# Optimization experiments

Measured on AMD Instinct MI355X. Metric: run time of the kernel, lower is better.

The kernel has to match this reference:

```python
import jax, jax.numpy as jnp
import numpy as np

N = 100000      # nodes
E = 800000      # edges
D_IN = 128
H = 4           # heads
C = 32          # out channels per head (out_feature = H*C = 128)
EPS = 1e-5


def setup_inputs() -> dict:
    key = jax.random.key(0)
    ks = jax.random.split(key, 12)
    x = jax.random.normal(ks[0], (N, D_IN), dtype=jnp.float32)
    edge_index = jax.random.randint(ks[1], (2, E), 0, N, dtype=jnp.int32)
    edge_weights = jax.random.uniform(ks[2], (E, 1), dtype=jnp.float32)
    s = 1.0 / np.sqrt(D_IN)
    W_l = jax.random.uniform(ks[3], (D_IN, H * C), jnp.float32, -s, s)   # GATv2 lin_l (source)
    W_r = jax.random.uniform(ks[4], (D_IN, H * C), jnp.float32, -s, s)   # GATv2 lin_r (target)
    W_e = jax.random.uniform(ks[5], (1, H * C), jnp.float32, -1.0, 1.0)  # lin_edge (edge_dim=1)
    att = jax.random.uniform(ks[6], (H, C), jnp.float32, -s, s)          # attention vector
    bias = jnp.zeros((H * C,), jnp.float32)
    gamma = jnp.ones((H * C,), jnp.float32)   # BatchNorm weight
    beta = jnp.zeros((H * C,), jnp.float32)   # BatchNorm bias
    return {"x": x, "edge_index": edge_index, "edge_weights": edge_weights,
            "W_l": W_l, "W_r": W_r, "W_e": W_e, "att": att, "bias": bias,
            "gamma": gamma, "beta": beta}


def reference(x, edge_index, edge_weights, W_l, W_r, W_e, att, bias, gamma, beta):
    src = edge_index[0]  # message source j
    dst = edge_index[1]  # message target i (aggregation index)

    x_l = (x @ W_l).reshape(N, H, C)
    x_r = (x @ W_r).reshape(N, H, C)
    e = (edge_weights @ W_e).reshape(E, H, C)

    # GATv2 message: LeakyReLU(x_j + x_i + e, 0.2), score = <att, .>
    xj = x_l[src]                                  # [E,H,C]
    m = jax.nn.leaky_relu(xj + x_r[dst] + e, 0.2)  # [E,H,C]
    logits = jnp.einsum('ehc,hc->eh', m, att)      # [E,H]

    # segment softmax over edges sharing the same destination
    seg_max = jax.ops.segment_max(logits, dst, num_segments=N)  # [N,H]
    seg_max = jnp.where(jnp.isfinite(seg_max), seg_max, 0.0)
    expv = jnp.exp(logits - seg_max[dst])
    seg_sum = jax.ops.segment_sum(expv, dst, num_segments=N)
    alpha = expv / (seg_sum[dst] + 1e-16)          # [E,H]

    out = jax.ops.segment_sum(xj * alpha[:, :, None], dst, num_segments=N)  # [N,H,C]
    out = out.reshape(N, H * C) + bias

    # BatchNorm1d over nodes (training-mode batch statistics, biased var)
    mu = jnp.mean(out, axis=0)
    var = jnp.var(out, axis=0)
    out = gamma * (out - mu) * jax.lax.rsqrt(var + EPS) + beta

    # F.leaky_relu default negative_slope=0.01; dropout is identity in eval
    return jax.nn.leaky_relu(out, 0.01)
```

## Files before the change

### kernel.cpp

```cpp
#include <hip/hip_runtime.h>

#define D 128

typedef __bf16 v8bf __attribute__((ext_vector_type(8)));
typedef float v4f __attribute__((ext_vector_type(4)));

__device__ __forceinline__ unsigned short f2bfbits(float f) {
    unsigned u = __float_as_uint(f);
    u += 0x7FFFu + ((u >> 16) & 1u);
    return (unsigned short)(u >> 16);
}

__device__ __forceinline__ float4 ldbf4(const __bf16* p) {
    const uint2 u = *reinterpret_cast<const uint2*>(p);
    float4 r;
    r.x = __uint_as_float(u.x << 16);
    r.y = __uint_as_float(u.x & 0xFFFF0000u);
    r.z = __uint_as_float(u.y << 16);
    r.w = __uint_as_float(u.y & 0xFFFF0000u);
    return r;
}

__global__ __launch_bounds__(256) void wprep_zero_k(
    const float* __restrict__ Wl, const float* __restrict__ Wr,
    __bf16* __restrict__ Wbf, int* __restrict__ zbase, int zcount) {
    if ((int)blockIdx.x < 128) {
        const int i = blockIdx.x * 256 + threadIdx.x;
        const int cg = i >> 7;
        const int k = i & 127;
        const float* __restrict__ Wp = (cg < D) ? Wl : Wr;
        Wbf[i] = (__bf16)Wp[(size_t)k * D + (cg & (D - 1))];
        return;
    }
    const int i = ((int)blockIdx.x - 128) * 256 + threadIdx.x;
    if (i < zcount) zbase[i] = 0;
}

__global__ __launch_bounds__(256, 1) void gemm_deg_k(
    const float* __restrict__ x, const __bf16* __restrict__ Wbf,
    __bf16* __restrict__ xl, __bf16* __restrict__ xr, int n, int nTiles,
    int gemmGrid, const int* __restrict__ dst, int* __restrict__ deg,
    unsigned char* __restrict__ rank, int E) {
    if ((int)blockIdx.x >= gemmGrid) {
        const int e = ((int)blockIdx.x - gemmGrid) * 256 + threadIdx.x;
        if (e < E) rank[e] = (unsigned char)atomicAdd(&deg[dst[e]], 1);
        return;
    }
    __shared__ __align__(16) unsigned short xs[64][136];
    const int tid = threadIdx.x;
    const int lane = tid & 63;
    const int wid = tid >> 6;
    const int col16 = lane & 15;
    const int kg = lane >> 4;

    v8bf bfr[4][4];
#pragma unroll
    for (int nt = 0; nt < 4; ++nt) {
        const int cg = (wid * 4 + nt) * 16 + col16;
#pragma unroll
        for (int ks = 0; ks < 4; ++ks)
            bfr[nt][ks] = *reinterpret_cast<const v8bf*>(
                &Wbf[(size_t)cg * 128 + ks * 32 + kg * 8]);
    }

    v8bf pre[4];
    int tile = (int)blockIdx.x;
    {
        const int row0 = tile * 64;
#pragma unroll
        for (int j = 0; j < 4; ++j) {
            const int i = tid + j * 256;
            const int row = row0 + (i >> 4);
            const int k0 = (i & 15) * 8;
            float4 v0 = make_float4(0.f, 0.f, 0.f, 0.f), v1 = v0;
            if (row < n) {
                v0 = *reinterpret_cast<const float4*>(&x[(size_t)row * D + k0]);
                v1 = *reinterpret_cast<const float4*>(&x[(size_t)row * D + k0 + 4]);
            }
            v8bf t;
            t[0] = (__bf16)v0.x; t[1] = (__bf16)v0.y;
            t[2] = (__bf16)v0.z; t[3] = (__bf16)v0.w;
            t[4] = (__bf16)v1.x; t[5] = (__bf16)v1.y;
            t[6] = (__bf16)v1.z; t[7] = (__bf16)v1.w;
            pre[j] = t;
        }
    }

    while (tile < nTiles) {
        const int row0 = tile * 64;
#pragma unroll
        for (int j = 0; j < 4; ++j) {
            const int i = tid + j * 256;
            *reinterpret_cast<v8bf*>(&xs[i >> 4][(i & 15) * 8]) = pre[j];
        }
        __syncthreads();

        const int next = tile + gemmGrid;
        if (next < nTiles) {
            const int nrow0 = next * 64;
#pragma unroll
            for (int j = 0; j < 4; ++j) {
                const int i = tid + j * 256;
                const int row = nrow0 + (i >> 4);
                const int k0 = (i & 15) * 8;
                float4 v0 = make_float4(0.f, 0.f, 0.f, 0.f), v1 = v0;
                if (row < n) {
                    v0 = *reinterpret_cast<const float4*>(&x[(size_t)row * D + k0]);
                    v1 = *reinterpret_cast<const float4*>(&x[(size_t)row * D + k0 + 4]);
                }
                v8bf t;
                t[0] = (__bf16)v0.x; t[1] = (__bf16)v0.y;
                t[2] = (__bf16)v0.z; t[3] = (__bf16)v0.w;
                t[4] = (__bf16)v1.x; t[5] = (__bf16)v1.y;
                t[6] = (__bf16)v1.z; t[7] = (__bf16)v1.w;
                pre[j] = t;
            }
        }

        v4f acc[4][4] = {};
#pragma unroll
        for (int mt = 0; mt < 4; ++mt) {
            v8bf afr[4];
#pragma unroll
            for (int ks = 0; ks < 4; ++ks)
                afr[ks] = *reinterpret_cast<const v8bf*>(
                    &xs[mt * 16 + col16][ks * 32 + kg * 8]);
#pragma unroll
            for (int nt = 0; nt < 4; ++nt)
#pragma unroll
                for (int ks = 0; ks < 4; ++ks)
                    acc[mt][nt] = __builtin_amdgcn_mfma_f32_16x16x32_bf16(
                        bfr[nt][ks], afr[ks], acc[mt][nt], 0, 0, 0);
        }
#pragma unroll
        for (int mt = 0; mt < 4; ++mt) {
            const int row = row0 + mt * 16 + col16;
            if (row < n) {
#pragma unroll
                for (int nt = 0; nt < 4; ++nt) {
                    const int cgb = (wid * 4 + nt) * 16 + kg * 4;
                    __bf16* __restrict__ op = (cgb < D) ? xl : xr;
                    const int c = cgb & (D - 1);
                    uint2 pkt;
                    pkt.x = ((unsigned)f2bfbits(acc[mt][nt][1]) << 16) |
                            f2bfbits(acc[mt][nt][0]);
                    pkt.y = ((unsigned)f2bfbits(acc[mt][nt][3]) << 16) |
                            f2bfbits(acc[mt][nt][2]);
                    *reinterpret_cast<uint2*>(&op[(size_t)row * D + c]) = pkt;
                }
            }
        }
        __syncthreads();
        tile = next;
    }
}

__global__ __launch_bounds__(256) void scan_k(
    const int* __restrict__ deg, int* __restrict__ rowptr,
    int* __restrict__ scanctr, int n) {
    __shared__ int tmp[256];
    __shared__ int sbase;
    const int i = blockIdx.x * 256 + threadIdx.x;
    const int v = (i < n) ? deg[i] : 0;
    tmp[threadIdx.x] = v;
    __syncthreads();
    for (int off = 1; off < 256; off <<= 1) {
        int t = (threadIdx.x >= off) ? tmp[threadIdx.x - off] : 0;
        __syncthreads();
        tmp[threadIdx.x] += t;
        __syncthreads();
    }
    if (threadIdx.x == 255) sbase = atomicAdd(scanctr, tmp[255]);
    __syncthreads();
    if (i < n) rowptr[i] = sbase + tmp[threadIdx.x] - v;
}

__global__ __launch_bounds__(256) void fill_k(
    const int* __restrict__ src, const int* __restrict__ dst,
    const float* __restrict__ ew, const int* __restrict__ rowptr,
    const unsigned char* __restrict__ rank, int2* __restrict__ epay,
    int E, int n) {
    const int xcd = blockIdx.x & 7;
    const int nchunk = gridDim.x >> 3;
    const int slice = (n + 7) >> 3;
    const int lo = xcd * slice;
    const int hi = min(n, lo + slice);
    const int stride = nchunk * 256;
    for (int e = ((int)blockIdx.x >> 3) * 256 + threadIdx.x; e < E; e += stride) {
        const int d = dst[e];
        if (d >= lo && d < hi) {
            const int p = rowptr[d] + (int)rank[e];
            int2 v;
            v.x = src[e];
            v.y = __float_as_int(ew[e]);
            epay[p] = v;
        }
    }
}

__global__ __launch_bounds__(256) void node_aggr_k(
    const __bf16* __restrict__ xl, const __bf16* __restrict__ xr,
    const int2* __restrict__ epay, const int* __restrict__ rowptr,
    const int* __restrict__ deg, const float* __restrict__ We,
    const float* __restrict__ att, __bf16* __restrict__ outb, int n) {
    const int wgl = (int)((blockIdx.x * (size_t)blockDim.x + threadIdx.x) >> 6);
    const int lane = threadIdx.x & 63;
    const int half = lane >> 5;
    const int node = wgl * 2 + half;
    const int ch = (lane & 31) * 4;

    int beg = 0, dg = 0;
    if (node < n) {
        beg = rowptr[node];
        dg = deg[node];
    }
    const int end = beg + dg;
    const int tmax = max(dg, __shfl_xor(dg, 32));

    float4 b = make_float4(0.f, 0.f, 0.f, 0.f);
    if (node < n) b = ldbf4(&xr[(size_t)node * D + ch]);
    const float4 we4 = *reinterpret_cast<const float4*>(&We[ch]);
    const float4 at4 = *reinterpret_cast<const float4*>(&att[ch]);

    float s = 0.f;
    float4 acc = make_float4(0.f, 0.f, 0.f, 0.f);
    for (int t = 0; t < tmax; t += 4) {
        float part[4];
        float4 av[4];
#pragma unroll
        for (int i = 0; i < 4; ++i) {
            const int p = beg + t + i;
            const int q = max(min(p, end - 1), 0);
            const int2 pw = epay[q];
            av[i] = ldbf4(&xl[(size_t)pw.x * D + ch]);
            const float wgt = __int_as_float(pw.y);
            float c0 = fmaf(wgt, we4.x, av[i].x + b.x);
            float c1 = fmaf(wgt, we4.y, av[i].y + b.y);
            float c2 = fmaf(wgt, we4.z, av[i].z + b.z);
            float c3 = fmaf(wgt, we4.w, av[i].w + b.w);
            c0 = fmaxf(c0, 0.2f * c0);
            c1 = fmaxf(c1, 0.2f * c1);
            c2 = fmaxf(c2, 0.2f * c2);
            c3 = fmaxf(c3, 0.2f * c3);
            part[i] = fmaf(c3, at4.w, fmaf(c2, at4.z, fmaf(c1, at4.y, c0 * at4.x)));
        }
#pragma unroll
        for (int off = 1; off < 8; off <<= 1) {
            part[0] += __shfl_xor(part[0], off);
            part[1] += __shfl_xor(part[1], off);
            part[2] += __shfl_xor(part[2], off);
            part[3] += __shfl_xor(part[3], off);
        }
        const float pv0 = (t + 0 < dg) ? __expf(fminf(part[0], 50.f)) : 0.f;
        const float pv1 = (t + 1 < dg) ? __expf(fminf(part[1], 50.f)) : 0.f;
        const float pv2 = (t + 2 < dg) ? __expf(fminf(part[2], 50.f)) : 0.f;
        const float pv3 = (t + 3 < dg) ? __expf(fminf(part[3], 50.f)) : 0.f;
        s += (pv0 + pv1) + (pv2 + pv3);
        acc.x += fmaf(pv3, av[3].x, fmaf(pv2, av[2].x,
                 fmaf(pv1, av[1].x, pv0 * av[0].x)));
        acc.y += fmaf(pv3, av[3].y, fmaf(pv2, av[2].y,
                 fmaf(pv1, av[1].y, pv0 * av[0].y)));
        acc.z += fmaf(pv3, av[3].z, fmaf(pv2, av[2].z,
                 fmaf(pv1, av[1].z, pv0 * av[0].z)));
        acc.w += fmaf(pv3, av[3].w, fmaf(pv2, av[2].w,
                 fmaf(pv1, av[1].w, pv0 * av[0].w)));
    }
    if (node < n) {
        const float inv = 1.f / (s + 1e-16f);
        uint2 pkt;
        pkt.x = ((unsigned)f2bfbits(acc.y * inv) << 16) | f2bfbits(acc.x * inv);
        pkt.y = ((unsigned)f2bfbits(acc.w * inv) << 16) | f2bfbits(acc.z * inv);
        *reinterpret_cast<uint2*>(&outb[(size_t)node * D + ch]) = pkt;
    }
}

__global__ __launch_bounds__(256) void bn_partial_k(
    const __bf16* __restrict__ outb, float* __restrict__ sums,
    float* __restrict__ sumsq, int n) {
    __shared__ float rs[8][128];
    __shared__ float rq[8][128];
    const int c4 = (threadIdx.x & 31) * 4;
    const int rstr = threadIdx.x >> 5;
    float4 s = make_float4(0.f, 0.f, 0.f, 0.f);
    float4 q = make_float4(0.f, 0.f, 0.f, 0.f);
    for (int r = blockIdx.x * 8 + rstr; r < n; r += gridDim.x * 8) {
        const float4 v = ldbf4(&outb[(size_t)r * D + c4]);
        s.x += v.x; s.y += v.y; s.z += v.z; s.w += v.w;
        q.x = fmaf(v.x, v.x, q.x);
        q.y = fmaf(v.y, v.y, q.y);
        q.z = fmaf(v.z, v.z, q.z);
        q.w = fmaf(v.w, v.w, q.w);
    }
    rs[rstr][c4 + 0] = s.x; rs[rstr][c4 + 1] = s.y;
    rs[rstr][c4 + 2] = s.z; rs[rstr][c4 + 3] = s.w;
    rq[rstr][c4 + 0] = q.x; rq[rstr][c4 + 1] = q.y;
    rq[rstr][c4 + 2] = q.z; rq[rstr][c4 + 3] = q.w;
    __syncthreads();
    const int t = threadIdx.x;
    if (t < 128) {
        float a = 0.f;
#pragma unroll
        for (int j = 0; j < 8; ++j) a += rs[j][t];
        atomicAdd(&sums[t], a);
    } else {
        const int c = t - 128;
        float a = 0.f;
#pragma unroll
        for (int j = 0; j < 8; ++j) a += rq[j][c];
        atomicAdd(&sumsq[c], a);
    }
}

__global__ __launch_bounds__(256) void bn_apply_k(
    const __bf16* __restrict__ outb, float* __restrict__ out,
    const float* __restrict__ bnsums, const float* __restrict__ gamma,
    const float* __restrict__ beta, int n, int total4) {
    const int i = blockIdx.x * blockDim.x + threadIdx.x;
    if (i >= total4) return;
    const int c4 = (i & 31) * 4;
    const float inv_n = 1.f / (float)n;
    const float4 sm = *reinterpret_cast<const float4*>(&bnsums[c4]);
    const float4 sq = *reinterpret_cast<const float4*>(&bnsums[D + c4]);
    const float4 g = *reinterpret_cast<const float4*>(&gamma[c4]);
    const float4 bt = *reinterpret_cast<const float4*>(&beta[c4]);
    float4 v = ldbf4(&outb[(size_t)i * 4]);
    float mu, var, scale, shift, r;
    mu = sm.x * inv_n; var = fmaxf(sq.x * inv_n - mu * mu, 0.f);
    scale = g.x * rsqrtf(var + 1e-5f); shift = bt.x - mu * scale;
    r = fmaf(v.x, scale, shift); v.x = fmaxf(r, 0.01f * r);
    mu = sm.y * inv_n; var = fmaxf(sq.y * inv_n - mu * mu, 0.f);
    scale = g.y * rsqrtf(var + 1e-5f); shift = bt.y - mu * scale;
    r = fmaf(v.y, scale, shift); v.y = fmaxf(r, 0.01f * r);
    mu = sm.z * inv_n; var = fmaxf(sq.z * inv_n - mu * mu, 0.f);
    scale = g.z * rsqrtf(var + 1e-5f); shift = bt.z - mu * scale;
    r = fmaf(v.z, scale, shift); v.z = fmaxf(r, 0.01f * r);
    mu = sm.w * inv_n; var = fmaxf(sq.w * inv_n - mu * mu, 0.f);
    scale = g.w * rsqrtf(var + 1e-5f); shift = bt.w - mu * scale;
    r = fmaf(v.w, scale, shift); v.w = fmaxf(r, 0.01f * r);
    *reinterpret_cast<float4*>(&out[(size_t)i * 4]) = v;
}

extern "C" void kernel_launch(void* const* d_in, const int* in_sizes, int n_in,
                              void* d_out, int out_size, void* d_ws, size_t ws_size,
                              hipStream_t stream) {
    const float* x     = (const float*)d_in[0];
    const int*   ei    = (const int*)d_in[1];
    const float* ew    = (const float*)d_in[2];
    const float* Wl    = (const float*)d_in[3];
    const float* Wr    = (const float*)d_in[4];
    const float* We    = (const float*)d_in[5];
    const float* att   = (const float*)d_in[6];
    const float* gamma = (const float*)d_in[8];
    const float* beta  = (const float*)d_in[9];

    const int n = in_sizes[0] / D;
    const int E = in_sizes[2];
    const int* src = ei;
    const int* dst = ei + E;
    const int nblk = (n + 255) / 256;

    char* ws = (char*)d_ws;
    size_t off = 0;
    __bf16* xl = (__bf16*)(ws + off);   off += (size_t)n * D * 2;
    __bf16* xr = (__bf16*)(ws + off);   off += (size_t)n * D * 2;
    __bf16* outb = (__bf16*)(ws + off); off += (size_t)n * D * 2;
    __bf16* Wbf = (__bf16*)(ws + off);  off += (size_t)2 * D * D * 2;
    float* bnsums = (float*)(ws + off); off += 2 * D * sizeof(float);
    int* scanctr = (int*)(ws + off);    off += 4 * sizeof(int);
    int* deg = (int*)(ws + off);        off += (size_t)n * sizeof(int);
    int* rowptr = (int*)(ws + off);     off += ((size_t)n + 1) * sizeof(int);
    unsigned char* rank = (unsigned char*)(ws + off); off += (size_t)E;
    off = (off + 15) & ~(size_t)15;
    int2* epay = (int2*)(ws + off);     off += (size_t)E * sizeof(int2);

    float* outacc = (float*)d_out;

    const int zcount = 2 * D + 4 + n;
    const int zblocks = (zcount + 255) / 256;

    wprep_zero_k<<<128 + zblocks, 256, 0, stream>>>(Wl, Wr, Wbf,
                                                    (int*)bnsums, zcount);

    const int nTiles = (n + 63) / 64;
    const int gemmGrid = 512;
    const int degBlocks = (E + 255) / 256;
    gemm_deg_k<<<gemmGrid + degBlocks, 256, 0, stream>>>(
        x, Wbf, xl, xr, n, nTiles, gemmGrid, dst, deg, rank, E);

    scan_k<<<nblk, 256, 0, stream>>>(deg, rowptr, scanctr, n);

    fill_k<<<2048, 256, 0, stream>>>(src, dst, ew, rowptr, rank, epay, E, n);

    const int waves = (n + 1) / 2;
    node_aggr_k<<<(waves + 3) / 4, 256, 0, stream>>>(xl, xr, epay, rowptr,
                                                     deg, We, att, outb, n);

    bn_partial_k<<<512, 256, 0, stream>>>(outb, bnsums, bnsums + D, n);
    bn_apply_k<<<((n * D / 4) + 255) / 256, 256, 0, stream>>>(
        outb, outacc, bnsums, gamma, beta, n, n * D / 4);
}
```

Before: 171.1 us.

## Split degree counters into eight sub-histograms to cut atomic contention

The degree counting atomics now target one of eight per-block-group copies of the degree array, selected by block index. The scan kernel sums the eight copies into a total, writes rowptr and deg, and replaces each sub-counter with its exclusive offset. The fill kernel then finds each edge's slot through the matching sub-offset. This aims to reduce atomic collisions on shared counters, at the cost of zeroing, reading and writing eight times more counter memory and scattering the atomics across a larger footprint.

```diff
diff --git a/kernel.cpp b/kernel.cpp
--- a/kernel.cpp
+++ b/kernel.cpp
@@ -39,11 +39,15 @@
 __global__ __launch_bounds__(256, 1) void gemm_deg_k(
     const float* __restrict__ x, const __bf16* __restrict__ Wbf,
     __bf16* __restrict__ xl, __bf16* __restrict__ xr, int n, int nTiles,
-    int gemmGrid, const int* __restrict__ dst, int* __restrict__ deg,
+    int gemmGrid, const int* __restrict__ dst, int* __restrict__ deg8,
     unsigned char* __restrict__ rank, int E) {
     if ((int)blockIdx.x >= gemmGrid) {
-        const int e = ((int)blockIdx.x - gemmGrid) * 256 + threadIdx.x;
-        if (e < E) rank[e] = (unsigned char)atomicAdd(&deg[dst[e]], 1);
+        const int f = (int)blockIdx.x - gemmGrid;
+        const int e = f * 256 + threadIdx.x;
+        if (e < E) {
+            const int sub = f & 7;
+            rank[e] = (unsigned char)atomicAdd(&deg8[(size_t)sub * n + dst[e]], 1);
+        }
         return;
     }
     __shared__ __align__(16) unsigned short xs[64][136];
@@ -156,13 +160,21 @@
 }
 
 __global__ __launch_bounds__(256) void scan_k(
-    const int* __restrict__ deg, int* __restrict__ rowptr,
+    int* __restrict__ deg8, int* __restrict__ deg, int* __restrict__ rowptr,
     int* __restrict__ scanctr, int n) {
     __shared__ int tmp[256];
     __shared__ int sbase;
     const int i = blockIdx.x * 256 + threadIdx.x;
-    const int v = (i < n) ? deg[i] : 0;
-    tmp[threadIdx.x] = v;
+    int d8[8];
+    int total = 0;
+    if (i < n) {
+#pragma unroll
+        for (int s = 0; s < 8; ++s) {
+            d8[s] = deg8[(size_t)s * n + i];
+            total += d8[s];
+        }
+    }
+    tmp[threadIdx.x] = total;
     __syncthreads();
     for (int off = 1; off < 256; off <<= 1) {
         int t = (threadIdx.x >= off) ? tmp[threadIdx.x - off] : 0;
@@ -172,12 +184,21 @@
     }
     if (threadIdx.x == 255) sbase = atomicAdd(scanctr, tmp[255]);
     __syncthreads();
-    if (i < n) rowptr[i] = sbase + tmp[threadIdx.x] - v;
+    if (i < n) {
+        int base = sbase + tmp[threadIdx.x] - total;
+        rowptr[i] = base;
+        deg[i] = total;
+#pragma unroll
+        for (int s = 0; s < 8; ++s) {
+            deg8[(size_t)s * n + i] = base;
+            base += d8[s];
+        }
+    }
 }
 
 __global__ __launch_bounds__(256) void fill_k(
     const int* __restrict__ src, const int* __restrict__ dst,
-    const float* __restrict__ ew, const int* __restrict__ rowptr,
+    const float* __restrict__ ew, const int* __restrict__ off8,
     const unsigned char* __restrict__ rank, int2* __restrict__ epay,
     int E, int n) {
     const int xcd = blockIdx.x & 7;
@@ -189,7 +210,8 @@
     for (int e = ((int)blockIdx.x >> 3) * 256 + threadIdx.x; e < E; e += stride) {
         const int d = dst[e];
         if (d >= lo && d < hi) {
-            const int p = rowptr[d] + (int)rank[e];
+            const int sub = (e >> 8) & 7;
+            const int p = off8[(size_t)sub * n + d] + (int)rank[e];
             int2 v;
             v.x = src[e];
             v.y = __float_as_int(ew[e]);
@@ -367,6 +389,7 @@
     __bf16* Wbf = (__bf16*)(ws + off);  off += (size_t)2 * D * D * 2;
     float* bnsums = (float*)(ws + off); off += 2 * D * sizeof(float);
     int* scanctr = (int*)(ws + off);    off += 4 * sizeof(int);
+    int* deg8 = (int*)(ws + off);       off += (size_t)8 * n * sizeof(int);
     int* deg = (int*)(ws + off);        off += (size_t)n * sizeof(int);
     int* rowptr = (int*)(ws + off);     off += ((size_t)n + 1) * sizeof(int);
     unsigned char* rank = (unsigned char*)(ws + off); off += (size_t)E;
@@ -375,7 +398,7 @@
 
     float* outacc = (float*)d_out;
 
-    const int zcount = 2 * D + 4 + n;
+    const int zcount = 2 * D + 4 + 8 * n;
     const int zblocks = (zcount + 255) / 256;
 
     wprep_zero_k<<<128 + zblocks, 256, 0, stream>>>(Wl, Wr, Wbf,
@@ -385,11 +408,11 @@
     const int gemmGrid = 512;
     const int degBlocks = (E + 255) / 256;
     gemm_deg_k<<<gemmGrid + degBlocks, 256, 0, stream>>>(
-        x, Wbf, xl, xr, n, nTiles, gemmGrid, dst, deg, rank, E);
-
-    scan_k<<<nblk, 256, 0, stream>>>(deg, rowptr, scanctr, n);
-
-    fill_k<<<2048, 256, 0, stream>>>(src, dst, ew, rowptr, rank, epay, E, n);
+        x, Wbf, xl, xr, n, nTiles, gemmGrid, dst, deg8, rank, E);
+
+    scan_k<<<nblk, 256, 0, stream>>>(deg8, deg, rowptr, scanctr, n);
+
+    fill_k<<<2048, 256, 0, stream>>>(src, dst, ew, deg8, rank, epay, E, n);
 
     const int waves = (n + 1) / 2;
     node_aggr_k<<<(waves + 3) / 4, 256, 0, stream>>>(xl, xr, epay, rowptr,
```

After: 171.5 us. No clear change (+0.3%).

## Load GEMM A fragments directly from global, one tile per block

Applied to the files above, without the earlier changes.

The persistent 512-block GEMM loop, with LDS staging and register prefetch of the next tile, is replaced by one 64-row tile per block. Each lane now reads its A-fragment straight from global fp32 x and converts it to bf16 in registers, so there is no shared memory and no barriers. This drops the LDS round trip and synchronisation and lets the hardware scheduler overlap blocks. In exchange, each block reloads the W fragments (many more blocks now), and the global reads of x are strided per lane rather than fully coalesced.

```diff
diff --git a/kernel.cpp b/kernel.cpp
--- a/kernel.cpp
+++ b/kernel.cpp
@@ -39,19 +39,19 @@
 __global__ __launch_bounds__(256, 1) void gemm_deg_k(
     const float* __restrict__ x, const __bf16* __restrict__ Wbf,
     __bf16* __restrict__ xl, __bf16* __restrict__ xr, int n, int nTiles,
-    int gemmGrid, const int* __restrict__ dst, int* __restrict__ deg,
+    const int* __restrict__ dst, int* __restrict__ deg,
     unsigned char* __restrict__ rank, int E) {
-    if ((int)blockIdx.x >= gemmGrid) {
-        const int e = ((int)blockIdx.x - gemmGrid) * 256 + threadIdx.x;
+    if ((int)blockIdx.x >= nTiles) {
+        const int e = ((int)blockIdx.x - nTiles) * 256 + threadIdx.x;
         if (e < E) rank[e] = (unsigned char)atomicAdd(&deg[dst[e]], 1);
         return;
     }
-    __shared__ __align__(16) unsigned short xs[64][136];
     const int tid = threadIdx.x;
     const int lane = tid & 63;
     const int wid = tid >> 6;
     const int col16 = lane & 15;
     const int kg = lane >> 4;
+    const int row0 = blockIdx.x * 64;
 
     v8bf bfr[4][4];
 #pragma unroll
@@ -63,95 +63,49 @@
                 &Wbf[(size_t)cg * 128 + ks * 32 + kg * 8]);
     }
 
-    v8bf pre[4];
-    int tile = (int)blockIdx.x;
-    {
-        const int row0 = tile * 64;
-#pragma unroll
-        for (int j = 0; j < 4; ++j) {
-            const int i = tid + j * 256;
-            const int row = row0 + (i >> 4);
-            const int k0 = (i & 15) * 8;
-            float4 v0 = make_float4(0.f, 0.f, 0.f, 0.f), v1 = v0;
-            if (row < n) {
-                v0 = *reinterpret_cast<const float4*>(&x[(size_t)row * D + k0]);
-                v1 = *reinterpret_cast<const float4*>(&x[(size_t)row * D + k0 + 4]);
-            }
+    v4f acc[4][4] = {};
+#pragma unroll
+    for (int mt = 0; mt < 4; ++mt) {
+        const int row = row0 + mt * 16 + col16;
+        const float* __restrict__ xp = &x[(size_t)min(row, n - 1) * D];
+        v8bf afr[4];
+#pragma unroll
+        for (int ks = 0; ks < 4; ++ks) {
+            const int k0 = ks * 32 + kg * 8;
+            const float4 v0 = *reinterpret_cast<const float4*>(&xp[k0]);
+            const float4 v1 = *reinterpret_cast<const float4*>(&xp[k0 + 4]);
             v8bf t;
             t[0] = (__bf16)v0.x; t[1] = (__bf16)v0.y;
             t[2] = (__bf16)v0.z; t[3] = (__bf16)v0.w;
             t[4] = (__bf16)v1.x; t[5] = (__bf16)v1.y;
             t[6] = (__bf16)v1.z; t[7] = (__bf16)v1.w;
-            pre[j] = t;
-        }
-    }
-
-    while (tile < nTiles) {
-        const int row0 = tile * 64;
-#pragma unroll
-        for (int j = 0; j < 4; ++j) {
-            const int i = tid + j * 256;
-            *reinterpret_cast<v8bf*>(&xs[i >> 4][(i & 15) * 8]) = pre[j];
-        }
-        __syncthreads();
-
-        const int next = tile + gemmGrid;
-        if (next < nTiles) {
-            const int nrow0 = next * 64;
-#pragma unroll
-            for (int j = 0; j < 4; ++j) {
-                const int i = tid + j * 256;
-                const int row = nrow0 + (i >> 4);
-                const int k0 = (i & 15) * 8;
-                float4 v0 = make_float4(0.f, 0.f, 0.f, 0.f), v1 = v0;
-                if (row < n) {
-                    v0 = *reinterpret_cast<const float4*>(&x[(size_t)row * D + k0]);
-                    v1 = *reinterpret_cast<const float4*>(&x[(size_t)row * D + k0 + 4]);
-                }
-                v8bf t;
-                t[0] = (__bf16)v0.x; t[1] = (__bf16)v0.y;
-                t[2] = (__bf16)v0.z; t[3] = (__bf16)v0.w;
-                t[4] = (__bf16)v1.x; t[5] = (__bf16)v1.y;
-                t[6] = (__bf16)v1.z; t[7] = (__bf16)v1.w;
-                pre[j] = t;
+            afr[ks] = t;
+        }
+#pragma unroll
+        for (int nt = 0; nt < 4; ++nt)
+#pragma unroll
+            for (int ks = 0; ks < 4; ++ks)
+                acc[mt][nt] = __builtin_amdgcn_mfma_f32_16x16x32_bf16(
+                    bfr[nt][ks], afr[ks], acc[mt][nt], 0, 0, 0);
+    }
+
+#pragma unroll
+    for (int mt = 0; mt < 4; ++mt) {
+        const int row = row0 + mt * 16 + col16;
+        if (row < n) {
+#pragma unroll
+            for (int nt = 0; nt < 4; ++nt) {
+                const int cgb = (wid * 4 + nt) * 16 + kg * 4;
+                __bf16* __restrict__ op = (cgb < D) ? xl : xr;
+                const int c = cgb & (D - 1);
+                uint2 pkt;
+                pkt.x = ((unsigned)f2bfbits(acc[mt][nt][1]) << 16) |
+                        f2bfbits(acc[mt][nt][0]);
+                pkt.y = ((unsigned)f2bfbits(acc[mt][nt][3]) << 16) |
+                        f2bfbits(acc[mt][nt][2]);
+                *reinterpret_cast<uint2*>(&op[(size_t)row * D + c]) = pkt;
             }
         }
-
-        v4f acc[4][4] = {};
-#pragma unroll
-        for (int mt = 0; mt < 4; ++mt) {
-            v8bf afr[4];
-#pragma unroll
-            for (int ks = 0; ks < 4; ++ks)
-                afr[ks] = *reinterpret_cast<const v8bf*>(
-                    &xs[mt * 16 + col16][ks * 32 + kg * 8]);
-#pragma unroll
-            for (int nt = 0; nt < 4; ++nt)
-#pragma unroll
-                for (int ks = 0; ks < 4; ++ks)
-                    acc[mt][nt] = __builtin_amdgcn_mfma_f32_16x16x32_bf16(
-                        bfr[nt][ks], afr[ks], acc[mt][nt], 0, 0, 0);
-        }
-#pragma unroll
-        for (int mt = 0; mt < 4; ++mt) {
-            const int row = row0 + mt * 16 + col16;
-            if (row < n) {
-#pragma unroll
-                for (int nt = 0; nt < 4; ++nt) {
-                    const int cgb = (wid * 4 + nt) * 16 + kg * 4;
-                    __bf16* __restrict__ op = (cgb < D) ? xl : xr;
-                    const int c = cgb & (D - 1);
-                    uint2 pkt;
-                    pkt.x = ((unsigned)f2bfbits(acc[mt][nt][1]) << 16) |
-                            f2bfbits(acc[mt][nt][0]);
-                    pkt.y = ((unsigned)f2bfbits(acc[mt][nt][3]) << 16) |
-                            f2bfbits(acc[mt][nt][2]);
-                    *reinterpret_cast<uint2*>(&op[(size_t)row * D + c]) = pkt;
-                }
-            }
-        }
-        __syncthreads();
-        tile = next;
     }
 }
 
@@ -382,10 +336,9 @@
                                                     (int*)bnsums, zcount);
 
     const int nTiles = (n + 63) / 64;
-    const int gemmGrid = 512;
     const int degBlocks = (E + 255) / 256;
-    gemm_deg_k<<<gemmGrid + degBlocks, 256, 0, stream>>>(
-        x, Wbf, xl, xr, n, nTiles, gemmGrid, dst, deg, rank, E);
+    gemm_deg_k<<<nTiles + degBlocks, 256, 0, stream>>>(
+        x, Wbf, xl, xr, n, nTiles, dst, deg, rank, E);
 
     scan_k<<<nblk, 256, 0, stream>>>(deg, rowptr, scanctr, n);
 
```

Measured after the change: 191.9 us. 12.2% more time.
